# Optimization experiments

Hardware: AMD Instinct MI355X
Metric: run time of the kernel (lower is better)

Reference implementation:

```python
import jax, jax.numpy as jnp
import numpy as np

B, QL, KVL = 2, 1024, 2048
D = 4096          # hidden_size
NH, NKV = 32, 8   # attention heads / kv heads
HD = D // NH      # head_dim = 128
INNER = 4 * D     # SwiGLU intermediate = 16384
EPS = 1e-5
THETA = 10000.0


def rope_cos_sin(seq_len, head_dim, theta):
    inv_freq = 1.0 / (theta ** (jnp.arange(0, head_dim, 2, dtype=jnp.float32) / head_dim))
    t = jnp.arange(seq_len, dtype=jnp.float32)
    freqs = jnp.outer(t, inv_freq)                      # [S, HD/2]
    emb = jnp.concatenate([freqs, freqs], axis=-1)      # [S, HD]
    return jnp.cos(emb), jnp.sin(emb)


def rotate_half(x):
    half = x.shape[-1] // 2
    return jnp.concatenate([-x[..., half:], x[..., :half]], axis=-1)


def apply_rope(x, cos, sin):
    # x: [B, H, S, HD]; cos/sin: [S, HD] broadcast over batch & heads
    return x * cos[None, None] + rotate_half(x) * sin[None, None]


def layernorm(x, w, b):
    mu = jnp.mean(x, axis=-1, keepdims=True)
    var = jnp.var(x, axis=-1, keepdims=True)
    return (x - mu) * jax.lax.rsqrt(var + EPS) * w + b


def setup_inputs() -> dict:
    key = jax.random.key(0)
    ks = jax.random.split(key, 12)
    s = 0.02
    return {
        "hidden_states": jax.random.normal(ks[0], (B, QL, D), jnp.float32),
        "encoder_hidden_states": jax.random.normal(ks[1], (B, KVL, D), jnp.float32),
        "encoder_attention_mask": jnp.ones((B, KVL), jnp.float32),
        "ln1_w": jnp.ones((D,), jnp.float32),
        "ln1_b": jnp.zeros((D,), jnp.float32),
        "q_w": jax.random.normal(ks[2], (D, D), jnp.float32) * s,        # [out, in]
        "k_w": jax.random.normal(ks[3], (NKV * HD, D), jnp.float32) * s,
        "v_w": jax.random.normal(ks[4], (NKV * HD, D), jnp.float32) * s,
        "o_w": jax.random.normal(ks[5], (D, D), jnp.float32) * s,
        "ln2_w": jnp.ones((D,), jnp.float32),
        "ln2_b": jnp.zeros((D,), jnp.float32),
        "gate_w": jax.random.normal(ks[6], (INNER, D), jnp.float32) * s,
        "up_w": jax.random.normal(ks[7], (INNER, D), jnp.float32) * s,
        "down_w": jax.random.normal(ks[8], (D, INNER), jnp.float32) * s,
    }


def reference(hidden_states, encoder_hidden_states, encoder_attention_mask,
              ln1_w, ln1_b, q_w, k_w, v_w, o_w, ln2_w, ln2_b,
              gate_w, up_w, down_w):
    residual = hidden_states
    h = layernorm(hidden_states, ln1_w, ln1_b)

    # projections
    q = (h @ q_w.T).reshape(B, QL, NH, HD).transpose(0, 2, 1, 3)                    # [B,NH,QL,HD]
    k = (encoder_hidden_states @ k_w.T).reshape(B, KVL, NKV, HD).transpose(0, 2, 1, 3)  # [B,NKV,KVL,HD]
    v = (encoder_hidden_states @ v_w.T).reshape(B, KVL, NKV, HD).transpose(0, 2, 1, 3)

    # RoPE: q uses positions 0..QL-1, k uses positions 0..KVL-1 (position_ids=None -> cos[None])
    q_cos, q_sin = rope_cos_sin(QL, HD, THETA)
    kv_cos, kv_sin = rope_cos_sin(KVL, HD, THETA)
    q = apply_rope(q, q_cos, q_sin)
    k = apply_rope(k, kv_cos, kv_sin)

    # GQA repeat_kv: each kv head repeated num_key_value_groups times consecutively
    n_rep = NH // NKV
    k = jnp.repeat(k, n_rep, axis=1)  # [B,NH,KVL,HD]
    v = jnp.repeat(v, n_rep, axis=1)

    attn = jnp.einsum('bhqd,bhkd->bhqk', q, k) / np.sqrt(HD).astype(np.float32)
    # NOTE: original code ADDS the boolean mask (True -> +1.0) to the logits
    mask = (encoder_attention_mask != 0).astype(attn.dtype)  # [B,KVL]
    attn = attn + mask[:, None, None, :]
    attn = jax.nn.softmax(attn.astype(jnp.float32), axis=-1).astype(q.dtype)

    out = jnp.einsum('bhqk,bhkd->bhqd', attn, v)        # [B,NH,QL,HD]
    out = out.transpose(0, 2, 1, 3).reshape(B, QL, D)
    attn_out = out @ o_w.T

    h = residual + attn_out
    residual = h
    h = layernorm(h, ln2_w, ln2_b)
    ff = (jax.nn.silu(h @ gate_w.T) * (h @ up_w.T)) @ down_w.T
    return residual + ff
```

## Files before the change

kernel.cpp:

```cpp
#include <hip/hip_runtime.h>
#include <hip/hip_bf16.h>
#include <math.h>

using bf16 = __hip_bfloat16;
typedef __bf16 bfv8 __attribute__((ext_vector_type(8)));
typedef float f32x4 __attribute__((ext_vector_type(4)));

__device__ __forceinline__ f32x4 mfma16(bfv8 a, bfv8 b, f32x4 c) {
    return __builtin_amdgcn_mfma_f32_16x16x32_bf16(a, b, c, 0, 0, 0);
}

__device__ __forceinline__ void gload_lds16(const void* g, void* l) {
    __builtin_amdgcn_global_load_lds(
        (const __attribute__((address_space(1))) void*)g,
        (__attribute__((address_space(3))) void*)l, 16, 0, 0);
}

__global__ void cvt_kernel(const float* __restrict__ in, bf16* __restrict__ out, long n8) {
    long u = (long)blockIdx.x * 256 + threadIdx.x;
    if (u >= n8) return;
    const float4* p = (const float4*)in + u * 2;
    float4 a = p[0], b = p[1];
    bf16 t8[8] = { __float2bfloat16(a.x), __float2bfloat16(a.y), __float2bfloat16(a.z), __float2bfloat16(a.w),
                   __float2bfloat16(b.x), __float2bfloat16(b.y), __float2bfloat16(b.z), __float2bfloat16(b.w) };
    *(int4*)(out + u * 8) = *(const int4*)t8;
}

__global__ void layernorm_kernel(const float* __restrict__ x, const float* __restrict__ gw,
                                 const float* __restrict__ gb, bf16* __restrict__ out)
{
    const int D = 4096;
    int row = blockIdx.x, t = threadIdx.x;
    const float4* xr = (const float4*)(x + (size_t)row * D);
    float4 v[4];
    float s1 = 0.f, s2 = 0.f;
#pragma unroll
    for (int j = 0; j < 4; ++j) {
        v[j] = xr[t + j * 256];
        s1 += v[j].x + v[j].y + v[j].z + v[j].w;
        s2 += v[j].x * v[j].x + v[j].y * v[j].y + v[j].z * v[j].z + v[j].w * v[j].w;
    }
#pragma unroll
    for (int d = 1; d < 64; d <<= 1) { s1 += __shfl_xor(s1, d); s2 += __shfl_xor(s2, d); }
    __shared__ float red[8];
    int wave = t >> 6, lane = t & 63;
    if (lane == 0) { red[wave] = s1; red[4 + wave] = s2; }
    __syncthreads();
    s1 = red[0] + red[1] + red[2] + red[3];
    s2 = red[4] + red[5] + red[6] + red[7];
    float mu = s1 * (1.f / 4096.f);
    float var = s2 * (1.f / 4096.f) - mu * mu;
    float rs = rsqrtf(var + 1e-5f);
    bf16* orow = out + (size_t)row * D;
#pragma unroll
    for (int j = 0; j < 4; ++j) {
        int base = (t + j * 256) * 4;
        float xs[4] = { v[j].x, v[j].y, v[j].z, v[j].w };
        bf16 o4[4];
#pragma unroll
        for (int c = 0; c < 4; ++c)
            o4[c] = __float2bfloat16((xs[c] - mu) * rs * gw[base + c] + gb[base + c]);
        *(int2*)(orow + base) = *(const int2*)o4;
    }
}

__global__ void rope_kernel(bf16* __restrict__ x, int nheads, int seqlen, long total) {
    long idx = (long)blockIdx.x * 256 + threadIdx.x;
    if (idx >= total) return;
    int j = (int)(idx & 63);
    long t2 = idx >> 6;
    int h = (int)(t2 % nheads);
    long row = t2 / nheads;
    int pos = (int)(row % seqlen);
    float inv = exp2f(-(float)j * 0.20762050593046015f);
    float ang = (float)pos * inv;
    float s, c;
    sincosf(ang, &s, &c);
    bf16* p = x + row * ((long)nheads * 128) + (long)h * 128 + j;
    float x0 = __bfloat162float(p[0]);
    float x1 = __bfloat162float(p[64]);
    p[0]  = __float2bfloat16(x0 * c - x1 * s);
    p[64] = __float2bfloat16(x1 * c + x0 * s);
}

template<int BM, int BN, int MODE, bool DUAL, int CM, int CN, int XN>
__global__ __launch_bounds__(512, 2) void gemm_p(
        const bf16* __restrict__ A, const bf16* __restrict__ W, const bf16* __restrict__ W2,
        void* __restrict__ Cout, void* __restrict__ Cout2, const void* __restrict__ aux,
        int M, int N, int K, int Nsplit)
{
    constexpr int MF = BM / 32;
    constexpr int NF = BN / 64;
    constexpr int ALD = BM / 128;
    constexpr int BLD = BN / 128;
    constexpr int SLD = ALD + BLD;
    __shared__ bf16 lds[3][(BM + BN) * 32];

    const int t = threadIdx.x;
    const int wid = t >> 6, lane = t & 63;
    const int lr = lane & 15, lg = lane >> 4;
    const int wr = wid >> 2, wc = wid & 3;
    const int bid = blockIdx.x;
    const int xcd = bid & 7, slot = bid >> 3;
    const int sm = slot / CN, sn = slot % CN;
    const int xm = xcd / XN, xn = xcd % XN;
    const int bm = (xm * CM + sm) * BM;
    const int bn = (xn * CN + sn) * BN;

    auto stage = [&](int tt, int buf) {
        const int k0 = tt * 32;
        char* ldsA = (char*)&lds[buf][0];
#pragma unroll
        for (int c = 0; c < ALD; ++c) {
            int Wb = (t + c * 512) * 16;
            int L = Wb ^ (((Wb >> 7) & 7) << 4);
            int row = L >> 6, colb = L & 63;
            gload_lds16(A + (size_t)(bm + row) * K + k0 + (colb >> 1), ldsA + Wb);
        }
        char* ldsB = (char*)&lds[buf][BM * 32];
#pragma unroll
        for (int c = 0; c < BLD; ++c) {
            int Wb = (t + c * 512) * 16;
            int L = Wb ^ (((Wb >> 7) & 7) << 4);
            int row = L >> 6, colb = L & 63;
            const bf16* src;
            if constexpr (DUAL) {
                int nr = bn + row;
                src = (nr >= Nsplit) ? W2 + (size_t)(nr - Nsplit) * K + k0 + (colb >> 1)
                                     : W  + (size_t)nr * K + k0 + (colb >> 1);
            } else {
                src = W + (size_t)(bn + row) * K + k0 + (colb >> 1);
            }
            gload_lds16(src, ldsB + Wb);
        }
    };

    const f32x4 zero4 = { 0.f, 0.f, 0.f, 0.f };
    f32x4 acc[MF][NF];
#pragma unroll
    for (int m = 0; m < MF; ++m)
#pragma unroll
        for (int n = 0; n < NF; ++n) acc[m][n] = zero4;

    const int T = K >> 5;
    stage(0, 0);
    stage(1, 1);
    if constexpr (SLD == 4) asm volatile("s_waitcnt vmcnt(4)" ::: "memory");
    else                    asm volatile("s_waitcnt vmcnt(3)" ::: "memory");
    __builtin_amdgcn_s_barrier();
    __builtin_amdgcn_sched_barrier(0);

    for (int tt = 0; tt < T; ++tt) {
        const int buf = tt % 3;
        bfv8 af[MF], bfr[NF];
#pragma unroll
        for (int m = 0; m < MF; ++m) {
            int row = wr * (BM / 2) + m * 16 + lr;
            int U = row * 64 + lg * 16;
            af[m] = *(const bfv8*)((const char*)&lds[buf][0] + (U ^ (((U >> 7) & 7) << 4)));
        }
#pragma unroll
        for (int n = 0; n < NF; ++n) {
            int row = wc * (BN / 4) + n * 16 + lr;
            int U = row * 64 + lg * 16;
            bfr[n] = *(const bfv8*)((const char*)&lds[buf][BM * 32] + (U ^ (((U >> 7) & 7) << 4)));
        }
        if (tt + 2 < T) stage(tt + 2, (tt + 2) % 3);
        __builtin_amdgcn_s_setprio(1);
#pragma unroll
        for (int m = 0; m < MF; ++m)
#pragma unroll
            for (int n = 0; n < NF; ++n)
                acc[m][n] = mfma16(af[m], bfr[n], acc[m][n]);
        __builtin_amdgcn_s_setprio(0);
        if (tt + 2 < T) {
            if constexpr (SLD == 4) asm volatile("s_waitcnt vmcnt(4)" ::: "memory");
            else                    asm volatile("s_waitcnt vmcnt(3)" ::: "memory");
        } else {
            asm volatile("s_waitcnt vmcnt(0)" ::: "memory");
        }
        __builtin_amdgcn_s_barrier();
        __builtin_amdgcn_sched_barrier(0);
    }

    const int r0 = bm + wr * (BM / 2), c0 = bn + wc * (BN / 4);
#pragma unroll
    for (int m = 0; m < MF; ++m)
#pragma unroll
        for (int n = 0; n < NF; ++n)
#pragma unroll
            for (int i = 0; i < 4; ++i) {
                int r = r0 + m * 16 + lg * 4 + i;
                int c = c0 + n * 16 + lr;
                float a = acc[m][n][i];
                if constexpr (DUAL) {
                    if (c < Nsplit) ((bf16*)Cout)[(size_t)r * Nsplit + c] = __float2bfloat16(a);
                    else ((bf16*)Cout2)[(size_t)r * (N - Nsplit) + (c - Nsplit)] = __float2bfloat16(a);
                } else {
                    size_t idx = (size_t)r * N + c;
                    if constexpr (MODE == 0) {
                        ((bf16*)Cout)[idx] = __float2bfloat16(a);
                    } else if constexpr (MODE == 1) {
                        a = a / (1.f + expf(-a));
                        ((bf16*)Cout)[idx] = __float2bfloat16(a);
                    } else if constexpr (MODE == 2) {
                        a *= __bfloat162float(((const bf16*)aux)[idx]);
                        ((bf16*)Cout)[idx] = __float2bfloat16(a);
                    } else {
                        ((float*)Cout)[idx] = a + ((const float*)aux)[idx];
                    }
                }
            }
}

template<int BN, int MODE, bool DUAL, int CM, int CN, int XN>
__global__ __launch_bounds__(512, 1) void gemm8(
        const bf16* __restrict__ A, const bf16* __restrict__ W, const bf16* __restrict__ W2,
        void* __restrict__ Cout, void* __restrict__ Cout2, const void* __restrict__ aux,
        int M, int N, int K, int Nsplit)
{
    constexpr bool BIG = (BN == 256);
    constexpr int NBUF = BIG ? 2 : 3;
    constexpr int ABY = 32768;
    constexpr int BBY = BN * 128;
    constexpr int TBY = ABY + BBY;
    __shared__ alignas(16) char lds8[NBUF * TBY];

    const int t = threadIdx.x;
    const int wid = t >> 6, lane = t & 63;
    const int lr = lane & 15, lg = lane >> 4;
    const int wr = wid >> 2, wc = wid & 3;
    const int bid = blockIdx.x;
    const int xcd = bid & 7, slot = bid >> 3;
    const int sm = slot / CN, sn = slot % CN;
    const int xm = xcd / XN, xn = xcd % XN;
    const int bm = (xm * CM + sm) * 256;
    const int bn = (xn * CN + sn) * BN;

    auto stA = [&](int kt, int h, int buf) {
#pragma unroll
        for (int c = 0; c < 2; ++c) {
            int Wb = (t + c * 512) * 16;
            int L = Wb ^ (((Wb >> 7) & 7) << 4);
            gload_lds16(A + (size_t)(bm + h * 128 + (L >> 7)) * K + kt * 64 + ((L & 127) >> 1),
                        lds8 + buf * TBY + h * 16384 + Wb);
        }
    };
    auto stB = [&](int kt, int h, int buf) {
#pragma unroll
        for (int c = 0; c < 2; ++c) {
            int Wb = (t + c * 512) * 16;
            int L = Wb ^ (((Wb >> 7) & 7) << 4);
            int nr = bn + h * 128 + (L >> 7);
            const bf16* src;
            if constexpr (DUAL) {
                src = (nr >= Nsplit) ? W2 + (size_t)(nr - Nsplit) * K + kt * 64 + ((L & 127) >> 1)
                                     : W  + (size_t)nr * K + kt * 64 + ((L & 127) >> 1);
            } else {
                src = W + (size_t)nr * K + kt * 64 + ((L & 127) >> 1);
            }
            gload_lds16(src, lds8 + buf * TBY + ABY + h * 16384 + Wb);
        }
    };

    const f32x4 zero4 = { 0.f, 0.f, 0.f, 0.f };
    f32x4 acc[8][BIG ? 4 : 2];
#pragma unroll
    for (int m = 0; m < 8; ++m)
#pragma unroll
        for (int n = 0; n < (BIG ? 4 : 2); ++n) acc[m][n] = zero4;

    bfv8 af[4][2], bfr[BIG ? 2 : 1][2][2];

#define LOADA(BUF, MH) do {                                                   \
    const char* _ba = lds8 + (BUF) * TBY;                                     \
    _Pragma("unroll") for (int m = 0; m < 4; ++m)                             \
    _Pragma("unroll") for (int ks = 0; ks < 2; ++ks) {                        \
        int row = wr * 128 + (MH) * 64 + m * 16 + lr;                         \
        int U = row * 128 + ks * 64 + lg * 16;                                \
        af[m][ks] = *(const bfv8*)(_ba + (U ^ ((row & 7) << 4)));             \
    } } while (0)

#define LOADB(BUF, NH) do {                                                   \
    const char* _bb = lds8 + (BUF) * TBY + ABY;                               \
    _Pragma("unroll") for (int n = 0; n < 2; ++n)                             \
    _Pragma("unroll") for (int ks = 0; ks < 2; ++ks) {                        \
        int row = wc * (BN / 4) + (NH) * (BN / 8) + n * 16 + lr;              \
        int U = row * 128 + ks * 64 + lg * 16;                                \
        bfr[NH][n][ks] = *(const bfv8*)(_bb + (U ^ ((row & 7) << 4)));        \
    } } while (0)

#define MFMAQ(MH, NH) do {                                                    \
    _Pragma("unroll") for (int m = 0; m < 4; ++m)                             \
    _Pragma("unroll") for (int n = 0; n < 2; ++n) {                           \
        acc[(MH)*4+m][(NH)*2+n] = mfma16(af[m][0], bfr[NH][n][0], acc[(MH)*4+m][(NH)*2+n]); \
        acc[(MH)*4+m][(NH)*2+n] = mfma16(af[m][1], bfr[NH][n][1], acc[(MH)*4+m][(NH)*2+n]); \
    } } while (0)

#define PH_TOP() do { __builtin_amdgcn_s_barrier();                           \
    asm volatile("s_waitcnt lgkmcnt(0)" ::: "memory");                        \
    __builtin_amdgcn_sched_barrier(0);                                        \
    __builtin_amdgcn_s_setprio(1); } while (0)

#define PH_END() do { __builtin_amdgcn_s_setprio(0);                          \
    __builtin_amdgcn_s_barrier(); } while (0)

#define GATE(LIVE) do { __builtin_amdgcn_s_setprio(0);                        \
    if (LIVE) { if constexpr (BIG) asm volatile("s_waitcnt vmcnt(4)" ::: "memory"); \
                else               asm volatile("s_waitcnt vmcnt(6)" ::: "memory"); } \
    else      asm volatile("s_waitcnt vmcnt(0)" ::: "memory");                \
    __builtin_amdgcn_s_barrier(); } while (0)

    const int T = K >> 6;
    const int T2 = T >> 1;

    if constexpr (BIG) {
        stA(0, 0, 0); stA(0, 1, 0); stB(0, 0, 0); stB(0, 1, 0);
        stB(1, 0, 1); stB(1, 1, 1);
        asm volatile("s_waitcnt vmcnt(4)" ::: "memory");
        __builtin_amdgcn_s_barrier();

        for (int tt = 0; tt < T2; ++tt) {
            const int o = 2 * tt + 1, e2 = 2 * tt + 2, o2 = 2 * tt + 3;
            const bool le = (e2 < T), lo = (o2 < T);
            LOADA(0, 0); LOADB(0, 0); stA(o, 0, 1);
            PH_TOP(); MFMAQ(0, 0); PH_END();
            LOADB(0, 1); stA(o, 1, 1);
            PH_TOP(); MFMAQ(0, 1); PH_END();
            LOADA(0, 1); if (le) stB(e2, 0, 0);
            PH_TOP(); MFMAQ(1, 1); PH_END();
            if (le) stB(e2, 1, 0);
            PH_TOP(); MFMAQ(1, 0); GATE(le);
            LOADA(1, 0); LOADB(1, 0); if (le) stA(e2, 0, 0);
            PH_TOP(); MFMAQ(0, 0); PH_END();
            LOADB(1, 1); if (le) stA(e2, 1, 0);
            PH_TOP(); MFMAQ(0, 1); PH_END();
            LOADA(1, 1); if (lo) stB(o2, 0, 1);
            PH_TOP(); MFMAQ(1, 1); PH_END();
            if (lo) stB(o2, 1, 1);
            PH_TOP(); MFMAQ(1, 0); GATE(le);
        }
    } else {
        stA(0, 0, 0); stB(0, 0, 0); stA(0, 1, 0);
        stA(1, 0, 1); stB(1, 0, 1); stA(1, 1, 1);
        asm volatile("s_waitcnt vmcnt(6)" ::: "memory");
        __builtin_amdgcn_s_barrier();

        int bE = 0, bO = 1, bN = 2;
        for (int tt = 0; tt < T2; ++tt) {
            const int e2 = 2 * tt + 2, o2 = 2 * tt + 3;
            const bool le = (e2 < T), lo = (o2 < T);
            LOADA(bE, 0); LOADB(bE, 0); if (le) { stA(e2, 0, bN); stB(e2, 0, bN); }
            PH_TOP(); MFMAQ(0, 0); PH_END();
            LOADA(bE, 1); if (le) stA(e2, 1, bN);
            PH_TOP(); MFMAQ(1, 0); GATE(le);
            LOADA(bO, 0); LOADB(bO, 0); if (lo) { stA(o2, 0, bE); stB(o2, 0, bE); }
            PH_TOP(); MFMAQ(0, 0); PH_END();
            LOADA(bO, 1); if (lo) stA(o2, 1, bE);
            PH_TOP(); MFMAQ(1, 0); GATE(lo);
            int nE = bN, nO = bE, nN = bO;
            bE = nE; bO = nO; bN = nN;
        }
    }

#undef LOADA
#undef LOADB
#undef MFMAQ
#undef PH_TOP
#undef PH_END
#undef GATE

    const int r0 = bm + wr * 128, c0 = bn + wc * (BN / 4);
#pragma unroll
    for (int mg = 0; mg < 8; ++mg)
#pragma unroll
        for (int ng = 0; ng < (BIG ? 4 : 2); ++ng)
#pragma unroll
            for (int i = 0; i < 4; ++i) {
                int r = r0 + mg * 16 + lg * 4 + i;
                int c = c0 + ng * 16 + lr;
                float a = acc[mg][ng][i];
                if constexpr (DUAL) {
                    if (c < Nsplit) ((bf16*)Cout)[(size_t)r * Nsplit + c] = __float2bfloat16(a);
                    else ((bf16*)Cout2)[(size_t)r * (N - Nsplit) + (c - Nsplit)] = __float2bfloat16(a);
                } else {
                    size_t idx = (size_t)r * N + c;
                    if constexpr (MODE == 0) {
                        ((bf16*)Cout)[idx] = __float2bfloat16(a);
                    } else if constexpr (MODE == 1) {
                        a = a / (1.f + expf(-a));
                        ((bf16*)Cout)[idx] = __float2bfloat16(a);
                    } else if constexpr (MODE == 2) {
                        a *= __bfloat162float(((const bf16*)aux)[idx]);
                        ((bf16*)Cout)[idx] = __float2bfloat16(a);
                    } else {
                        ((float*)Cout)[idx] = a + ((const float*)aux)[idx];
                    }
                }
            }
}

__global__ void transpose_v(const bf16* __restrict__ vb, bf16* __restrict__ vt) {
    __shared__ bf16 tile[64][68];
    int kv0 = blockIdx.x * 64, c0 = blockIdx.y * 64, b = blockIdx.z;
    int t = threadIdx.x;
    int cr = t & 15, rr = t >> 4;
#pragma unroll
    for (int j = 0; j < 4; ++j) {
        int r = rr + j * 16;
        *(int2*)&tile[r][cr * 4] = *(const int2*)&vb[(size_t)(b * 2048 + kv0 + r) * 1024 + c0 + cr * 4];
    }
    __syncthreads();
#pragma unroll
    for (int j = 0; j < 4; ++j) {
        int cc = rr + j * 16;
        bf16 tmp[4];
#pragma unroll
        for (int q = 0; q < 4; ++q) tmp[q] = tile[cr * 4 + q][cc];
        *(int2*)&vt[(size_t)(b * 1024 + c0 + cc) * 2048 + kv0 + cr * 4] = *(const int2*)tmp;
    }
}

__global__ __launch_bounds__(256) void attn_kernel(
    const bf16* __restrict__ Q, const bf16* __restrict__ Kb, const bf16* __restrict__ Vt,
    const float* __restrict__ mask, bf16* __restrict__ O)
{
    const int QL_ = 1024, KVL_ = 2048;
    const float scale = 0.08838834764831845f;
    int qt = blockIdx.x, h = blockIdx.y, b = blockIdx.z;
    int t = threadIdx.x, wave = t >> 6, lane = t & 63;
    int lr = lane & 15, lg = lane >> 4;
    int g = h >> 2;
    __shared__ bf16 Ksm[64 * 128];
    __shared__ bf16 Vsm[128 * 64];
    __shared__ bf16 Psm[4][16 * 72];
    int q0 = qt * 64 + wave * 16;

    const bf16* qptr = Q + (size_t)(b * QL_ + q0 + lr) * 4096 + h * 128;
    bfv8 qf[4];
#pragma unroll
    for (int kc = 0; kc < 4; ++kc) qf[kc] = *(const bfv8*)(qptr + kc * 32 + lg * 8);

    const f32x4 zero4 = { 0.f, 0.f, 0.f, 0.f };
    f32x4 accO[8];
#pragma unroll
    for (int dt = 0; dt < 8; ++dt) accO[dt] = zero4;
    float mrow[4] = { -1e30f, -1e30f, -1e30f, -1e30f };
    float lrow[4] = { 0.f, 0.f, 0.f, 0.f };

    for (int kv0 = 0; kv0 < KVL_; kv0 += 64) {
#pragma unroll
        for (int p2 = 0; p2 < 4; ++p2) {
            int Wb = (p2 * 256 + t) * 16;
            int row = Wb >> 8;
            int col = ((Wb & 255) ^ ((row & 7) << 4)) >> 1;
            gload_lds16(Kb + (size_t)(b * KVL_ + kv0 + row) * 1024 + g * 128 + col,
                        (char*)Ksm + Wb);
        }
#pragma unroll
        for (int p2 = 0; p2 < 4; ++p2) {
            int Wb = (p2 * 256 + t) * 16;
            int row = Wb >> 7;
            int col = ((Wb & 127) ^ ((row & 7) << 4)) >> 1;
            gload_lds16(Vt + (size_t)(b * 1024 + g * 128 + row) * 2048 + kv0 + col,
                        (char*)Vsm + Wb);
        }
        __syncthreads();

        f32x4 s[4];
#pragma unroll
        for (int ct = 0; ct < 4; ++ct) {
            s[ct] = zero4;
#pragma unroll
            for (int kc = 0; kc < 4; ++kc) {
                int row = ct * 16 + lr;
                int U = row * 256 + kc * 64 + lg * 16;
                bfv8 kf = *(const bfv8*)((const char*)Ksm + (U ^ ((row & 7) << 4)));
                s[ct] = mfma16(qf[kc], kf, s[ct]);
            }
            float mv = mask[(size_t)b * KVL_ + kv0 + ct * 16 + lr];
            mv = (mv != 0.f) ? 1.f : 0.f;
#pragma unroll
            for (int i = 0; i < 4; ++i) s[ct][i] = s[ct][i] * scale + mv;
        }

        float rmx[4], mnew[4], corr[4], psum[4];
#pragma unroll
        for (int i = 0; i < 4; ++i) {
            rmx[i] = fmaxf(fmaxf(s[0][i], s[1][i]), fmaxf(s[2][i], s[3][i]));
#pragma unroll
            for (int d = 1; d < 16; d <<= 1) rmx[i] = fmaxf(rmx[i], __shfl_xor(rmx[i], d));
            mnew[i] = fmaxf(mrow[i], rmx[i]);
            corr[i] = expf(mrow[i] - mnew[i]);
            psum[i] = 0.f;
        }
#pragma unroll
        for (int ct = 0; ct < 4; ++ct)
#pragma unroll
            for (int i = 0; i < 4; ++i) {
                float pv = expf(s[ct][i] - mnew[i]);
                psum[i] += pv;
                Psm[wave][(lg * 4 + i) * 72 + ct * 16 + lr] = __float2bfloat16(pv);
            }
#pragma unroll
        for (int i = 0; i < 4; ++i) {
#pragma unroll
            for (int d = 1; d < 16; d <<= 1) psum[i] += __shfl_xor(psum[i], d);
            lrow[i] = lrow[i] * corr[i] + psum[i];
            mrow[i] = mnew[i];
        }
#pragma unroll
        for (int dt = 0; dt < 8; ++dt)
#pragma unroll
            for (int i = 0; i < 4; ++i) accO[dt][i] *= corr[i];
        __syncthreads();

        bfv8 pf0 = *(const bfv8*)&Psm[wave][lr * 72 + 0 * 32 + lg * 8];
        bfv8 pf1 = *(const bfv8*)&Psm[wave][lr * 72 + 1 * 32 + lg * 8];
#pragma unroll
        for (int dt = 0; dt < 8; ++dt) {
            int row = dt * 16 + lr;
            int U0 = row * 128 + 0 * 64 + lg * 16;
            int U1 = row * 128 + 1 * 64 + lg * 16;
            bfv8 vf0 = *(const bfv8*)((const char*)Vsm + (U0 ^ ((row & 7) << 4)));
            bfv8 vf1 = *(const bfv8*)((const char*)Vsm + (U1 ^ ((row & 7) << 4)));
            accO[dt] = mfma16(pf0, vf0, accO[dt]);
            accO[dt] = mfma16(pf1, vf1, accO[dt]);
        }
        __syncthreads();
    }

    float invl[4];
#pragma unroll
    for (int i = 0; i < 4; ++i) invl[i] = 1.f / lrow[i];
#pragma unroll
    for (int dt = 0; dt < 8; ++dt)
#pragma unroll
        for (int i = 0; i < 4; ++i)
            O[(size_t)(b * QL_ + q0 + lg * 4 + i) * 4096 + h * 128 + dt * 16 + lr] =
                __float2bfloat16(accO[dt][i] * invl[i]);
}

extern "C" void kernel_launch(void* const* d_in, const int* in_sizes, int n_in,
                              void* d_out, int out_size, void* d_ws, size_t ws_size,
                              hipStream_t stream) {
    const float* hidden = (const float*)d_in[0];
    const float* enc    = (const float*)d_in[1];
    const float* mask   = (const float*)d_in[2];
    const float* ln1w   = (const float*)d_in[3];
    const float* ln1b   = (const float*)d_in[4];
    const float* qw     = (const float*)d_in[5];
    const float* kw     = (const float*)d_in[6];
    const float* vw     = (const float*)d_in[7];
    const float* ow     = (const float*)d_in[8];
    const float* ln2w   = (const float*)d_in[9];
    const float* ln2b   = (const float*)d_in[10];
    const float* gatew  = (const float*)d_in[11];
    const float* upw    = (const float*)d_in[12];
    const float* downw  = (const float*)d_in[13];
    float* out = (float*)d_out;

    char* ws = (char*)d_ws;
    bf16*  wbuf  = (bf16*)(ws);
    bf16*  wbuf2 = (bf16*)(ws + 8388608);
    bf16*  h1    = (bf16*)(ws + 134217728);
    bf16*  encb  = (bf16*)(ws + 150994944);
    bf16*  qb    = (bf16*)(ws + 184549376);
    bf16*  kb    = (bf16*)(ws + 201326592);
    bf16*  vb    = (bf16*)(ws + 209715200);
    bf16*  attno = (bf16*)(ws + 218103808);
    float* h2    = (float*)(ws + 234881024);
    bf16*  vt    = (bf16*)(ws + 234881024);
    bf16*  h2n   = (bf16*)(ws + 268435456);
    bf16*  g1    = (bf16*)(ws + 285212672);

    auto cvt = [&](const float* src, bf16* dst, long n) {
        cvt_kernel<<<(int)(n / 2048), 256, 0, stream>>>(src, dst, n / 8);
    };

    cvt(enc, encb, 16777216L);
    layernorm_kernel<<<2048, 256, 0, stream>>>(hidden, ln1w, ln1b, h1);

    cvt(qw, wbuf, 16777216L);
    gemm_p<128, 256, 0, false, 8, 4, 4><<<256, 512, 0, stream>>>(
        h1, wbuf, nullptr, qb, nullptr, nullptr, 2048, 4096, 4096, 0);
    rope_kernel<<<16384, 256, 0, stream>>>(qb, 32, 1024, 2048L * 32 * 64);

    cvt(kw, wbuf, 4194304L);
    cvt(vw, wbuf2, 4194304L);
    gemm_p<128, 256, 0, true, 8, 4, 2><<<256, 512, 0, stream>>>(
        encb, wbuf, wbuf2, kb, vb, nullptr, 4096, 2048, 4096, 1024);
    rope_kernel<<<8192, 256, 0, stream>>>(kb, 8, 2048, 4096L * 8 * 64);
    transpose_v<<<dim3(32, 16, 2), 256, 0, stream>>>(vb, vt);

    attn_kernel<<<dim3(16, 32, 2), 256, 0, stream>>>(qb, kb, vt, mask, attno);

    cvt(ow, wbuf, 16777216L);
    gemm_p<128, 256, 3, false, 8, 4, 4><<<256, 512, 0, stream>>>(
        attno, wbuf, nullptr, h2, nullptr, hidden, 2048, 4096, 4096, 0);

    layernorm_kernel<<<2048, 256, 0, stream>>>(h2, ln2w, ln2b, h2n);

    cvt(gatew, wbuf, 67108864L);
    gemm8<256, 1, false, 8, 8, 8><<<512, 512, 0, stream>>>(
        h2n, wbuf, nullptr, g1, nullptr, nullptr, 2048, 16384, 4096, 0);
    cvt(upw, wbuf, 67108864L);
    gemm8<256, 2, false, 8, 8, 8><<<512, 512, 0, stream>>>(
        h2n, wbuf, nullptr, g1, nullptr, g1, 2048, 16384, 4096, 0);

    cvt(downw, wbuf, 67108864L);
    gemm8<128, 3, false, 8, 4, 8><<<256, 512, 0, stream>>>(
        g1, wbuf, nullptr, out, nullptr, h2, 2048, 4096, 16384, 0);
}
```

Before: 1.490 ms.

## Double-buffer attention K/V tiles and reshape small-tile GEMM wave layout

The attention kernel now stages the next K/V tile into a second LDS buffer while the current tile is being computed, using a vmcnt wait instead of a full sync. This hides global-to-LDS latency behind the QK and PV MFMAs. Separately, the BN=128 GEMM path changes its per-wave tiling from 2x4 waves (128x32 each) to 4x2 waves (64x64 each), which makes the per-wave output tile squarer so fragments are reused more. The costs are doubled LDS usage for attention and a removed barrier around the per-wave P buffer, which relies on each wave owning its own Psm slice.

```diff
diff --git a/kernel.cpp b/kernel.cpp
--- a/kernel.cpp
+++ b/kernel.cpp
@@ -229,7 +229,8 @@
     const int t = threadIdx.x;
     const int wid = t >> 6, lane = t & 63;
     const int lr = lane & 15, lg = lane >> 4;
-    const int wr = wid >> 2, wc = wid & 3;
+    const int wrB = wid >> 2, wcB = wid & 3;
+    const int wr4 = wid >> 1, wc4 = wid & 1;
     const int bid = blockIdx.x;
     const int xcd = bid & 7, slot = bid >> 3;
     const int sm = slot / CN, sn = slot % CN;
@@ -264,19 +265,20 @@
     };
 
     const f32x4 zero4 = { 0.f, 0.f, 0.f, 0.f };
-    f32x4 acc[8][BIG ? 4 : 2];
-#pragma unroll
-    for (int m = 0; m < 8; ++m)
-#pragma unroll
-        for (int n = 0; n < (BIG ? 4 : 2); ++n) acc[m][n] = zero4;
-
-    bfv8 af[4][2], bfr[BIG ? 2 : 1][2][2];
+    f32x4 acc[BIG ? 8 : 4][4];
+#pragma unroll
+    for (int m = 0; m < (BIG ? 8 : 4); ++m)
+#pragma unroll
+        for (int n = 0; n < 4; ++n) acc[m][n] = zero4;
+
+    bfv8 af[4][2], bfr[2][2][2];
+    bfv8 afs[2][2], bfs[4][2];
 
 #define LOADA(BUF, MH) do {                                                   \
     const char* _ba = lds8 + (BUF) * TBY;                                     \
     _Pragma("unroll") for (int m = 0; m < 4; ++m)                             \
     _Pragma("unroll") for (int ks = 0; ks < 2; ++ks) {                        \
-        int row = wr * 128 + (MH) * 64 + m * 16 + lr;                         \
+        int row = wrB * 128 + (MH) * 64 + m * 16 + lr;                        \
         int U = row * 128 + ks * 64 + lg * 16;                                \
         af[m][ks] = *(const bfv8*)(_ba + (U ^ ((row & 7) << 4)));             \
     } } while (0)
@@ -285,7 +287,7 @@
     const char* _bb = lds8 + (BUF) * TBY + ABY;                               \
     _Pragma("unroll") for (int n = 0; n < 2; ++n)                             \
     _Pragma("unroll") for (int ks = 0; ks < 2; ++ks) {                        \
-        int row = wc * (BN / 4) + (NH) * (BN / 8) + n * 16 + lr;              \
+        int row = wcB * 64 + (NH) * 32 + n * 16 + lr;                         \
         int U = row * 128 + ks * 64 + lg * 16;                                \
         bfr[NH][n][ks] = *(const bfv8*)(_bb + (U ^ ((row & 7) << 4)));        \
     } } while (0)
@@ -295,6 +297,31 @@
     _Pragma("unroll") for (int n = 0; n < 2; ++n) {                           \
         acc[(MH)*4+m][(NH)*2+n] = mfma16(af[m][0], bfr[NH][n][0], acc[(MH)*4+m][(NH)*2+n]); \
         acc[(MH)*4+m][(NH)*2+n] = mfma16(af[m][1], bfr[NH][n][1], acc[(MH)*4+m][(NH)*2+n]); \
+    } } while (0)
+
+#define LOADA_S(BUF, MH) do {                                                 \
+    const char* _ba = lds8 + (BUF) * TBY;                                     \
+    _Pragma("unroll") for (int m = 0; m < 2; ++m)                             \
+    _Pragma("unroll") for (int ks = 0; ks < 2; ++ks) {                        \
+        int row = wr4 * 64 + (MH) * 32 + m * 16 + lr;                         \
+        int U = row * 128 + ks * 64 + lg * 16;                                \
+        afs[m][ks] = *(const bfv8*)(_ba + (U ^ ((row & 7) << 4)));            \
+    } } while (0)
+
+#define LOADB_S(BUF) do {                                                     \
+    const char* _bb = lds8 + (BUF) * TBY + ABY;                               \
+    _Pragma("unroll") for (int n = 0; n < 4; ++n)                             \
+    _Pragma("unroll") for (int ks = 0; ks < 2; ++ks) {                        \
+        int row = wc4 * 64 + n * 16 + lr;                                     \
+        int U = row * 128 + ks * 64 + lg * 16;                                \
+        bfs[n][ks] = *(const bfv8*)(_bb + (U ^ ((row & 7) << 4)));            \
+    } } while (0)
+
+#define MFMAQ_S(MH) do {                                                      \
+    _Pragma("unroll") for (int m = 0; m < 2; ++m)                             \
+    _Pragma("unroll") for (int n = 0; n < 4; ++n) {                           \
+        acc[(MH)*2+m][n] = mfma16(afs[m][0], bfs[n][0], acc[(MH)*2+m][n]);    \
+        acc[(MH)*2+m][n] = mfma16(afs[m][1], bfs[n][1], acc[(MH)*2+m][n]);    \
     } } while (0)
 
 #define PH_TOP() do { __builtin_amdgcn_s_barrier();                           \
@@ -350,14 +377,14 @@
         for (int tt = 0; tt < T2; ++tt) {
             const int e2 = 2 * tt + 2, o2 = 2 * tt + 3;
             const bool le = (e2 < T), lo = (o2 < T);
-            LOADA(bE, 0); LOADB(bE, 0); if (le) { stA(e2, 0, bN); stB(e2, 0, bN); }
-            PH_TOP(); MFMAQ(0, 0); PH_END();
-            LOADA(bE, 1); if (le) stA(e2, 1, bN);
-            PH_TOP(); MFMAQ(1, 0); GATE(le);
-            LOADA(bO, 0); LOADB(bO, 0); if (lo) { stA(o2, 0, bE); stB(o2, 0, bE); }
-            PH_TOP(); MFMAQ(0, 0); PH_END();
-            LOADA(bO, 1); if (lo) stA(o2, 1, bE);
-            PH_TOP(); MFMAQ(1, 0); GATE(lo);
+            LOADA_S(bE, 0); LOADB_S(bE); if (le) { stA(e2, 0, bN); stB(e2, 0, bN); }
+            PH_TOP(); MFMAQ_S(0); PH_END();
+            LOADA_S(bE, 1); if (le) stA(e2, 1, bN);
+            PH_TOP(); MFMAQ_S(1); GATE(le);
+            LOADA_S(bO, 0); LOADB_S(bO); if (lo) { stA(o2, 0, bE); stB(o2, 0, bE); }
+            PH_TOP(); MFMAQ_S(0); PH_END();
+            LOADA_S(bO, 1); if (lo) stA(o2, 1, bE);
+            PH_TOP(); MFMAQ_S(1); GATE(lo);
             int nE = bN, nO = bE, nN = bO;
             bE = nE; bO = nO; bN = nN;
         }
@@ -366,15 +393,19 @@
 #undef LOADA
 #undef LOADB
 #undef MFMAQ
+#undef LOADA_S
+#undef LOADB_S
+#undef MFMAQ_S
 #undef PH_TOP
 #undef PH_END
 #undef GATE
 
-    const int r0 = bm + wr * 128, c0 = bn + wc * (BN / 4);
-#pragma unroll
-    for (int mg = 0; mg < 8; ++mg)
-#pragma unroll
-        for (int ng = 0; ng < (BIG ? 4 : 2); ++ng)
+    const int r0 = bm + (BIG ? wrB * 128 : wr4 * 64);
+    const int c0 = bn + (BIG ? wcB * 64 : wc4 * 64);
+#pragma unroll
+    for (int mg = 0; mg < (BIG ? 8 : 4); ++mg)
+#pragma unroll
+        for (int ng = 0; ng < 4; ++ng)
 #pragma unroll
             for (int i = 0; i < 4; ++i) {
                 int r = r0 + mg * 16 + lg * 4 + i;
@@ -431,31 +462,19 @@
     int t = threadIdx.x, wave = t >> 6, lane = t & 63;
     int lr = lane & 15, lg = lane >> 4;
     int g = h >> 2;
-    __shared__ bf16 Ksm[64 * 128];
-    __shared__ bf16 Vsm[128 * 64];
+    __shared__ bf16 Ksm[2][64 * 128];
+    __shared__ bf16 Vsm[2][128 * 64];
     __shared__ bf16 Psm[4][16 * 72];
     int q0 = qt * 64 + wave * 16;
 
-    const bf16* qptr = Q + (size_t)(b * QL_ + q0 + lr) * 4096 + h * 128;
-    bfv8 qf[4];
-#pragma unroll
-    for (int kc = 0; kc < 4; ++kc) qf[kc] = *(const bfv8*)(qptr + kc * 32 + lg * 8);
-
-    const f32x4 zero4 = { 0.f, 0.f, 0.f, 0.f };
-    f32x4 accO[8];
-#pragma unroll
-    for (int dt = 0; dt < 8; ++dt) accO[dt] = zero4;
-    float mrow[4] = { -1e30f, -1e30f, -1e30f, -1e30f };
-    float lrow[4] = { 0.f, 0.f, 0.f, 0.f };
-
-    for (int kv0 = 0; kv0 < KVL_; kv0 += 64) {
+    auto stage = [&](int buf, int kv0) {
 #pragma unroll
         for (int p2 = 0; p2 < 4; ++p2) {
             int Wb = (p2 * 256 + t) * 16;
             int row = Wb >> 8;
             int col = ((Wb & 255) ^ ((row & 7) << 4)) >> 1;
             gload_lds16(Kb + (size_t)(b * KVL_ + kv0 + row) * 1024 + g * 128 + col,
-                        (char*)Ksm + Wb);
+                        (char*)&Ksm[buf][0] + Wb);
         }
 #pragma unroll
         for (int p2 = 0; p2 < 4; ++p2) {
@@ -463,9 +482,34 @@
             int row = Wb >> 7;
             int col = ((Wb & 127) ^ ((row & 7) << 4)) >> 1;
             gload_lds16(Vt + (size_t)(b * 1024 + g * 128 + row) * 2048 + kv0 + col,
-                        (char*)Vsm + Wb);
-        }
-        __syncthreads();
+                        (char*)&Vsm[buf][0] + Wb);
+        }
+    };
+
+    const bf16* qptr = Q + (size_t)(b * QL_ + q0 + lr) * 4096 + h * 128;
+    bfv8 qf[4];
+#pragma unroll
+    for (int kc = 0; kc < 4; ++kc) qf[kc] = *(const bfv8*)(qptr + kc * 32 + lg * 8);
+
+    const f32x4 zero4 = { 0.f, 0.f, 0.f, 0.f };
+    f32x4 accO[8];
+#pragma unroll
+    for (int dt = 0; dt < 8; ++dt) accO[dt] = zero4;
+    float mrow[4] = { -1e30f, -1e30f, -1e30f, -1e30f };
+    float lrow[4] = { 0.f, 0.f, 0.f, 0.f };
+
+    stage(0, 0);
+    int buf = 0;
+    const int NT = KVL_ / 64;
+    for (int tt = 0; tt < NT; ++tt) {
+        const int kv0 = tt * 64;
+        if (tt + 1 < NT) {
+            stage(buf ^ 1, kv0 + 64);
+            asm volatile("s_waitcnt vmcnt(8)" ::: "memory");
+        } else {
+            asm volatile("s_waitcnt vmcnt(0)" ::: "memory");
+        }
+        __builtin_amdgcn_s_barrier();
 
         f32x4 s[4];
 #pragma unroll
@@ -475,7 +519,7 @@
             for (int kc = 0; kc < 4; ++kc) {
                 int row = ct * 16 + lr;
                 int U = row * 256 + kc * 64 + lg * 16;
-                bfv8 kf = *(const bfv8*)((const char*)Ksm + (U ^ ((row & 7) << 4)));
+                bfv8 kf = *(const bfv8*)((const char*)&Ksm[buf][0] + (U ^ ((row & 7) << 4)));
                 s[ct] = mfma16(qf[kc], kf, s[ct]);
             }
             float mv = mask[(size_t)b * KVL_ + kv0 + ct * 16 + lr];
@@ -513,7 +557,6 @@
         for (int dt = 0; dt < 8; ++dt)
 #pragma unroll
             for (int i = 0; i < 4; ++i) accO[dt][i] *= corr[i];
-        __syncthreads();
 
         bfv8 pf0 = *(const bfv8*)&Psm[wave][lr * 72 + 0 * 32 + lg * 8];
         bfv8 pf1 = *(const bfv8*)&Psm[wave][lr * 72 + 1 * 32 + lg * 8];
@@ -522,12 +565,13 @@
             int row = dt * 16 + lr;
             int U0 = row * 128 + 0 * 64 + lg * 16;
             int U1 = row * 128 + 1 * 64 + lg * 16;
-            bfv8 vf0 = *(const bfv8*)((const char*)Vsm + (U0 ^ ((row & 7) << 4)));
-            bfv8 vf1 = *(const bfv8*)((const char*)Vsm + (U1 ^ ((row & 7) << 4)));
+            bfv8 vf0 = *(const bfv8*)((const char*)&Vsm[buf][0] + (U0 ^ ((row & 7) << 4)));
+            bfv8 vf1 = *(const bfv8*)((const char*)&Vsm[buf][0] + (U1 ^ ((row & 7) << 4)));
             accO[dt] = mfma16(pf0, vf0, accO[dt]);
             accO[dt] = mfma16(pf1, vf1, accO[dt]);
         }
-        __syncthreads();
+        __builtin_amdgcn_s_barrier();
+        buf ^= 1;
     }
 
     float invl[4];
```

Measured after the change: 1.496 ms. No clear change (+0.4%).
